# Performance work log

Measured on AMD Instinct MI355X. Metric: run time of the kernel, lower is better.

Reference implementation:

```python
import jax, jax.numpy as jnp
import numpy as np

N, E, F_IN, H, T, G, NCONV = 50000, 800000, 128, 64, 8, 64, 3
BN_EPS = 1e-5


def _bn_relu(h, gamma, beta):
    # BatchNorm1d in training mode: biased batch stats over the node dim
    m = h.mean(axis=0)
    v = h.var(axis=0)
    return jax.nn.relu(gamma * (h - m) * jax.lax.rsqrt(v + BN_EPS) + beta)


def _mlp(h, W1, b1, g1, be1, W2, b2, g2, be2):
    h = _bn_relu(h @ W1 + b1, g1, be1)
    return _bn_relu(h @ W2 + b2, g2, be2)


def setup_inputs() -> dict:
    key = jax.random.key(0)
    ks = jax.random.split(key, 12)
    x = jax.random.normal(ks[0], (N, F_IN), dtype=jnp.float32)
    edge_index = jax.random.randint(ks[1], (2, E), 0, N, dtype=jnp.int64)
    batch = jnp.sort(jax.random.randint(ks[2], (N,), 0, G, dtype=jnp.int64))
    s = 0.05
    inp = {
        "x": x, "edge_index": edge_index, "batch": batch,
        # first_h: Linear(F_IN,H)+BN+ReLU+Linear(H,H)+BN+ReLU
        "fh_W1": jax.random.normal(ks[3], (F_IN, H), jnp.float32) * s,
        "fh_b1": jnp.zeros((H,), jnp.float32),
        "fh_g1": jnp.ones((H,), jnp.float32),
        "fh_be1": jnp.zeros((H,), jnp.float32),
        "fh_W2": jax.random.normal(ks[4], (H, H), jnp.float32) * s,
        "fh_b2": jnp.zeros((H,), jnp.float32),
        "fh_g2": jnp.ones((H,), jnp.float32),
        "fh_be2": jnp.zeros((H,), jnp.float32),
        # stacked GINConv MLPs (all H->H)
        "cv_W1": jax.random.normal(ks[5], (NCONV, H, H), jnp.float32) * s,
        "cv_b1": jnp.zeros((NCONV, H), jnp.float32),
        "cv_g1": jnp.ones((NCONV, H), jnp.float32),
        "cv_be1": jnp.zeros((NCONV, H), jnp.float32),
        "cv_W2": jax.random.normal(ks[6], (NCONV, H, H), jnp.float32) * s,
        "cv_b2": jnp.zeros((NCONV, H), jnp.float32),
        "cv_g2": jnp.ones((NCONV, H), jnp.float32),
        "cv_be2": jnp.zeros((NCONV, H), jnp.float32),
        # per-layer readout linears (NCONV+1 of them)
        "lin_W": jax.random.normal(ks[7], (NCONV + 1, H, T), jnp.float32) * s,
        "lin_b": jnp.zeros((NCONV + 1, T), jnp.float32),
    }
    return inp


def reference(x, edge_index, batch, fh_W1, fh_b1, fh_g1, fh_be1, fh_W2, fh_b2,
              fh_g2, fh_be2, cv_W1, cv_b1, cv_g1, cv_be1, cv_W2, cv_b2, cv_g2,
              cv_be2, lin_W, lin_b):
    src, dst = edge_index[0], edge_index[1]
    eps = 0.0  # eps=0.0, train_eps=False
    # layer 0: first_h + pooled readout
    h = _mlp(x, fh_W1, fh_b1, fh_g1, fh_be1, fh_W2, fh_b2, fh_g2, fh_be2)
    out = jax.ops.segment_max(h @ lin_W[0] + lin_b[0], batch, num_segments=G)
    # GIN conv layers: neighbor sum-aggregation + MLP, with per-layer readout
    for l in range(NCONV):
        agg = jax.ops.segment_sum(h[src], dst, num_segments=N)  # [N,H]
        h = _mlp((1.0 + eps) * h + agg, cv_W1[l], cv_b1[l], cv_g1[l],
                 cv_be1[l], cv_W2[l], cv_b2[l], cv_g2[l], cv_be2[l])
        out = out + jax.ops.segment_max(h @ lin_W[l + 1] + lin_b[l + 1],
                                        batch, num_segments=G)
    return (out, h)
```

## Files before the change

### kernel.cpp

```cpp
#include <hip/hip_runtime.h>
#include <hip/hip_fp16.h>

#define NN 50000
#define EE 800000
#define FIN 128
#define HH 64
#define TT 8
#define GG 64
#define NCONVS 3
#define BN_EPS 1e-5f
#define RNODES 64
#define NBKT 196
#define SCAT_CHUNK 2048

typedef _Float16 h2f __attribute__((ext_vector_type(2)));

__device__ __forceinline__ unsigned enc_f32(float x) {
  unsigned u = __float_as_uint(x);
  return (u & 0x80000000u) ? ~u : (u | 0x80000000u);
}
__device__ __forceinline__ float dec_f32(unsigned e) {
  unsigned u = (e & 0x80000000u) ? (e & 0x7fffffffu) : ~e;
  return __uint_as_float(u);
}

__device__ __forceinline__ float fdot2f(int a, int b, float c) {
#if __has_builtin(__builtin_amdgcn_fdot2)
  return __builtin_amdgcn_fdot2(__builtin_bit_cast(h2f, a),
                                __builtin_bit_cast(h2f, b), c, false);
#else
  const __half2 ha = __builtin_bit_cast(__half2, a);
  const __half2 hb = __builtin_bit_cast(__half2, b);
  const float2 fa = __half22float2(ha), fb = __half22float2(hb);
  return fmaf(fa.y, fb.y, fmaf(fa.x, fb.x, c));
#endif
}

template <int K, int MODE>
__global__ __launch_bounds__(128) void mm_stats_kernel(
    const float* __restrict__ in, const __half* __restrict__ hin,
    const __half* __restrict__ agg, const float* __restrict__ stats_in,
    const float* __restrict__ gamma, const float* __restrict__ beta,
    const float* __restrict__ W, const float* __restrict__ bias,
    __half* __restrict__ y16, float* __restrict__ stats_out) {
  constexpr int NPH = K / 64;
  __shared__ __half2 Wl2[(K / 2) * HH];
  __shared__ __half2 AT2[32 * 68];
  __shared__ float ssl[128];
  __shared__ float sred[2][128];
  const int t = threadIdx.x;
  if (MODE != 0) {
    if (t < 64) {
      const float inv = 1.f / (float)NN;
      const float mean = stats_in[t] * inv;
      const float var = stats_in[64 + t] * inv - mean * mean;
      const float sc = gamma[t] * rsqrtf(var + BN_EPS);
      ssl[t] = sc;
      ssl[64 + t] = fmaf(-mean, sc, beta[t]);
    }
    __syncthreads();
  }
#pragma unroll
  for (int i = 0; i < K / 4; ++i) {
    const int idx = t + i * 128;
    const int kk = idx >> 6, c = idx & 63;
    Wl2[idx] = __floats2half2_rn(W[(2 * kk) * HH + c], W[(2 * kk + 1) * HH + c]);
  }
  const int srow = t >> 1, shalf = t & 1;
  const int grow_s = blockIdx.x * 64 + srow;
  const int cg = t & 7, rg = t >> 3;
  const int c0 = cg * 8, r0 = rg * 4;
  float acc[4][8] = {};

#pragma unroll
  for (int p = 0; p < NPH; ++p) {
    if (p > 0) __syncthreads();
    if (grow_s < NN) {
      if (MODE == 0) {
#pragma unroll
        for (int q = 0; q < 4; ++q) {
          const int cc = p * 64 + shalf * 32 + q * 8;
          const float4 v0 = *(const float4*)&in[(size_t)grow_s * K + cc];
          const float4 v1 = *(const float4*)&in[(size_t)grow_s * K + cc + 4];
          const int kk = shalf * 16 + q * 4;
          AT2[(kk + 0) * 68 + srow] = __floats2half2_rn(v0.x, v0.y);
          AT2[(kk + 1) * 68 + srow] = __floats2half2_rn(v0.z, v0.w);
          AT2[(kk + 2) * 68 + srow] = __floats2half2_rn(v1.x, v1.y);
          AT2[(kk + 3) * 68 + srow] = __floats2half2_rn(v1.z, v1.w);
        }
      } else {
#pragma unroll
        for (int q = 0; q < 4; ++q) {
          const int cc = shalf * 32 + q * 8;
          const int4 rv = *(const int4*)&hin[grow_s * HH + cc];
          const __half2* hp = (const __half2*)&rv;
          float f[8];
          {
            const float2 f0 = __half22float2(hp[0]);
            const float2 f1 = __half22float2(hp[1]);
            const float2 f2 = __half22float2(hp[2]);
            const float2 f3 = __half22float2(hp[3]);
            f[0] = f0.x; f[1] = f0.y; f[2] = f1.x; f[3] = f1.y;
            f[4] = f2.x; f[5] = f2.y; f[6] = f3.x; f[7] = f3.y;
          }
#pragma unroll
          for (int j = 0; j < 8; ++j)
            f[j] = fmaxf(fmaf(f[j], ssl[cc + j], ssl[64 + cc + j]), 0.f);
          if (MODE == 2) {
            const int4 av = *(const int4*)&agg[grow_s * HH + cc];
            const __half2* ap = (const __half2*)&av;
            const float2 a0 = __half22float2(ap[0]);
            const float2 a1 = __half22float2(ap[1]);
            const float2 a2 = __half22float2(ap[2]);
            const float2 a3 = __half22float2(ap[3]);
            f[0] += a0.x; f[1] += a0.y; f[2] += a1.x; f[3] += a1.y;
            f[4] += a2.x; f[5] += a2.y; f[6] += a3.x; f[7] += a3.y;
          }
          const int kk = shalf * 16 + q * 4;
          AT2[(kk + 0) * 68 + srow] = __floats2half2_rn(f[0], f[1]);
          AT2[(kk + 1) * 68 + srow] = __floats2half2_rn(f[2], f[3]);
          AT2[(kk + 2) * 68 + srow] = __floats2half2_rn(f[4], f[5]);
          AT2[(kk + 3) * 68 + srow] = __floats2half2_rn(f[6], f[7]);
        }
      }
    } else {
      const __half2 z = __floats2half2_rn(0.f, 0.f);
#pragma unroll
      for (int i2 = 0; i2 < 16; ++i2) AT2[(shalf * 16 + i2) * 68 + srow] = z;
    }
    __syncthreads();
#pragma unroll 8
    for (int kk = 0; kk < 32; ++kk) {
      const int4 w0 = *(const int4*)&Wl2[(p * 32 + kk) * HH + c0];
      const int4 w1 = *(const int4*)&Wl2[(p * 32 + kk) * HH + c0 + 4];
      const int4 av = *(const int4*)&AT2[kk * 68 + r0];
      const int wu[8] = {w0.x, w0.y, w0.z, w0.w, w1.x, w1.y, w1.z, w1.w};
      const int au[4] = {av.x, av.y, av.z, av.w};
#pragma unroll
      for (int r = 0; r < 4; ++r)
#pragma unroll
        for (int c = 0; c < 8; ++c)
          acc[r][c] = fdot2f(au[r], wu[c], acc[r][c]);
    }
  }
  const float4 bb0 = *(const float4*)&bias[c0];
  const float4 bb1 = *(const float4*)&bias[c0 + 4];
  const float bbv[8] = {bb0.x, bb0.y, bb0.z, bb0.w, bb1.x, bb1.y, bb1.z, bb1.w};
  float st_s[8] = {}, st_q[8] = {};
  const int row0 = blockIdx.x * 64 + r0;
#pragma unroll
  for (int ri = 0; ri < 4; ++ri) {
    const int grow = row0 + ri;
    if (grow < NN) {
      float o[8];
#pragma unroll
      for (int c = 0; c < 8; ++c) {
        o[c] = acc[ri][c] + bbv[c];
        st_s[c] += o[c];
        st_q[c] = fmaf(o[c], o[c], st_q[c]);
      }
      const __half2 p0 = __floats2half2_rn(o[0], o[1]);
      const __half2 p1 = __floats2half2_rn(o[2], o[3]);
      const __half2 p2 = __floats2half2_rn(o[4], o[5]);
      const __half2 p3 = __floats2half2_rn(o[6], o[7]);
      int4 pk;
      pk.x = *(const int*)&p0; pk.y = *(const int*)&p1;
      pk.z = *(const int*)&p2; pk.w = *(const int*)&p3;
      *(int4*)&y16[grow * HH + c0] = pk;
    }
  }
#pragma unroll
  for (int off = 8; off <= 32; off <<= 1) {
#pragma unroll
    for (int c = 0; c < 8; ++c) {
      st_s[c] += __shfl_xor(st_s[c], off);
      st_q[c] += __shfl_xor(st_q[c], off);
    }
  }
  const int wave = t >> 6, lane = t & 63;
  if (lane < 8) {
#pragma unroll
    for (int c = 0; c < 8; ++c) {
      sred[wave][lane * 8 + c] = st_s[c];
      sred[wave][64 + lane * 8 + c] = st_q[c];
    }
  }
  __syncthreads();
  if (t < 128) atomicAdd(&stats_out[t], sred[0][t] + sred[1][t]);
}

__global__ __launch_bounds__(256) void bcount_kernel(const int* __restrict__ ei,
                                                     int* __restrict__ bcnt) {
  __shared__ int l[256];
  const int t = threadIdx.x;
  l[t] = 0;
  __syncthreads();
  for (int e = blockIdx.x * 256 + t; e < EE; e += gridDim.x * 256)
    atomicAdd(&l[ei[EE + e] >> 8], 1);
  __syncthreads();
  if (t < NBKT && l[t]) atomicAdd(&bcnt[t], l[t]);
}

__global__ void bscan_kernel(const int* __restrict__ bcnt,
                             int* __restrict__ bbase, int* __restrict__ bcur) {
  __shared__ int s[256];
  const int t = threadIdx.x;
  const int v = (t < NBKT) ? bcnt[t] : 0;
  s[t] = v;
  __syncthreads();
  for (int off = 1; off < 256; off <<= 1) {
    const int u = (t >= off) ? s[t - off] : 0;
    __syncthreads();
    s[t] += u;
    __syncthreads();
  }
  const int excl = s[t] - v;
  if (t < NBKT) {
    bbase[t] = excl;
    bcur[t] = excl;
  }
  if (t == 255) bbase[NBKT] = s[255];
}

__global__ __launch_bounds__(256) void bscatter_kernel(
    const int* __restrict__ ei, int* __restrict__ bcur,
    unsigned long long* __restrict__ ebuf) {
  __shared__ int lcnt[256];
  __shared__ int lbase[256];
  const int t = threadIdx.x;
  lcnt[t] = 0;
  __syncthreads();
  const int e0 = blockIdx.x * SCAT_CHUNK;
  int mysrc[8], mydl[8], mybkt[8], myloc[8];
#pragma unroll
  for (int i = 0; i < 8; ++i) {
    const int e = e0 + i * 256 + t;
    if (e < EE) {
      const int dst = ei[EE + e];
      mybkt[i] = dst >> 8;
      mydl[i] = dst & 255;
      mysrc[i] = ei[e];
      myloc[i] = atomicAdd(&lcnt[mybkt[i]], 1);
    } else {
      mybkt[i] = -1;
    }
  }
  __syncthreads();
  if (t < NBKT && lcnt[t]) lbase[t] = atomicAdd(&bcur[t], lcnt[t]);
  __syncthreads();
#pragma unroll
  for (int i = 0; i < 8; ++i) {
    if (mybkt[i] >= 0) {
      const int pos = lbase[mybkt[i]] + myloc[i];
      ebuf[pos] = ((unsigned long long)(unsigned)mydl[i] << 32) |
                  (unsigned)mysrc[i];
    }
  }
}

__global__ __launch_bounds__(256) void bcsr_kernel(
    const int* __restrict__ bbase, const unsigned long long* __restrict__ ebuf,
    int* __restrict__ offs, int* __restrict__ srcs) {
  __shared__ int ldeg[256];
  __shared__ int sscan[256];
  __shared__ int lcur[256];
  const int t = threadIdx.x;
  const int b = blockIdx.x;
  const int e0 = bbase[b], e1 = bbase[b + 1];
  ldeg[t] = 0;
  __syncthreads();
  for (int e = e0 + t; e < e1; e += 256)
    atomicAdd(&ldeg[(int)(ebuf[e] >> 32)], 1);
  __syncthreads();
  const int v = ldeg[t];
  sscan[t] = v;
  __syncthreads();
  for (int off = 1; off < 256; off <<= 1) {
    const int u = (t >= off) ? sscan[t - off] : 0;
    __syncthreads();
    sscan[t] += u;
    __syncthreads();
  }
  const int excl = sscan[t] - v;
  const int node = b * 256 + t;
  if (node < NN) offs[node] = e0 + excl;
  if (b == NBKT - 1 && t == 0) offs[NN] = EE;
  lcur[t] = e0 + excl;
  __syncthreads();
  for (int e = e0 + t; e < e1; e += 256) {
    const unsigned long long u = ebuf[e];
    const int dl = (int)(u >> 32);
    const int pos = atomicAdd(&lcur[dl], 1);
    srcs[pos] = (int)(u & 0xffffffffu);
  }
}

__global__ __launch_bounds__(256) void gather16_kernel(
    const int* __restrict__ offs, const int* __restrict__ srcs,
    const __half* __restrict__ y, const float* __restrict__ stats_in,
    const float* __restrict__ gamma, const float* __restrict__ beta,
    __half* __restrict__ agg) {
  __shared__ float ssl[128];
  const int t = threadIdx.x;
  if (t < 64) {
    const float inv = 1.f / (float)NN;
    const float mean = stats_in[t] * inv;
    const float var = stats_in[64 + t] * inv - mean * mean;
    const float sc = gamma[t] * rsqrtf(var + BN_EPS);
    ssl[t] = sc;
    ssl[64 + t] = fmaf(-mean, sc, beta[t]);
  }
  __syncthreads();
  const int gid = blockIdx.x * 256 + t;
  const int n = gid >> 3, lane = gid & 7;
  if (n >= NN) return;
  const int c0 = lane * 8;
  float sc[8], sh[8];
#pragma unroll
  for (int j = 0; j < 8; ++j) {
    sc[j] = ssl[c0 + j];
    sh[j] = ssl[64 + c0 + j];
  }
  const int s0 = offs[n], s1 = offs[n + 1];
  float a[8] = {};
#pragma unroll 2
  for (int j = s0; j < s1; ++j) {
    const int4 rv = *(const int4*)&y[srcs[j] * HH + c0];
    const __half2* hp = (const __half2*)&rv;
    const float2 f0 = __half22float2(hp[0]);
    const float2 f1 = __half22float2(hp[1]);
    const float2 f2 = __half22float2(hp[2]);
    const float2 f3 = __half22float2(hp[3]);
    a[0] += fmaxf(fmaf(f0.x, sc[0], sh[0]), 0.f);
    a[1] += fmaxf(fmaf(f0.y, sc[1], sh[1]), 0.f);
    a[2] += fmaxf(fmaf(f1.x, sc[2], sh[2]), 0.f);
    a[3] += fmaxf(fmaf(f1.y, sc[3], sh[3]), 0.f);
    a[4] += fmaxf(fmaf(f2.x, sc[4], sh[4]), 0.f);
    a[5] += fmaxf(fmaf(f2.y, sc[5], sh[5]), 0.f);
    a[6] += fmaxf(fmaf(f3.x, sc[6], sh[6]), 0.f);
    a[7] += fmaxf(fmaf(f3.y, sc[7], sh[7]), 0.f);
  }
  const __half2 p0 = __floats2half2_rn(a[0], a[1]);
  const __half2 p1 = __floats2half2_rn(a[2], a[3]);
  const __half2 p2 = __floats2half2_rn(a[4], a[5]);
  const __half2 p3 = __floats2half2_rn(a[6], a[7]);
  int4 pk;
  pk.x = *(const int*)&p0; pk.y = *(const int*)&p1;
  pk.z = *(const int*)&p2; pk.w = *(const int*)&p3;
  *(int4*)&agg[n * HH + c0] = pk;
}

template <int WMODE>
__global__ __launch_bounds__(256) void bnrelu_readout_kernel(
    const __half* __restrict__ y2, const float* __restrict__ stats_in,
    const float* __restrict__ gamma, const float* __restrict__ beta,
    float* __restrict__ hout, const float* __restrict__ linW,
    const float* __restrict__ linb, const int* __restrict__ batch,
    unsigned* __restrict__ outmax) {
  __shared__ float Wl[HH * 9];
  __shared__ float lb[8];
  __shared__ float ssl[128];
  __shared__ unsigned smax[8][8];
  const int t = threadIdx.x;
  if (t < 64) {
#pragma unroll
    for (int j = 0; j < 8; ++j) Wl[t * 9 + j] = linW[t * 8 + j];
    const float inv = 1.f / (float)NN;
    const float mean = stats_in[t] * inv;
    const float var = stats_in[64 + t] * inv - mean * mean;
    const float sc = gamma[t] * rsqrtf(var + BN_EPS);
    ssl[t] = sc;
    ssl[64 + t] = fmaf(-mean, sc, beta[t]);
  }
  if (t < 8) lb[t] = linb[t];
  if (t >= 64 && t < 128) smax[(t - 64) >> 3][(t - 64) & 7] = 0u;
  const int gfirst = batch[blockIdx.x * RNODES < NN ? blockIdx.x * RNODES : NN - 1];
  __syncthreads();
  const int nl = t >> 3;
  const int c0 = (t & 7) * 8;
  const int b0 = t & 1, b1 = (t >> 1) & 1, b2 = (t >> 2) & 1;
#pragma unroll
  for (int chunk = 0; chunk < RNODES / 32; ++chunk) {
    const int n = blockIdx.x * RNODES + chunk * 32 + nl;
    if (n < NN) {
      float hv[8];
      {
        const int4 rv = *(const int4*)&y2[n * HH + c0];
        const __half2* hp = (const __half2*)&rv;
        const float2 f0 = __half22float2(hp[0]);
        const float2 f1 = __half22float2(hp[1]);
        const float2 f2 = __half22float2(hp[2]);
        const float2 f3 = __half22float2(hp[3]);
        hv[0] = fmaxf(fmaf(f0.x, ssl[c0 + 0], ssl[64 + c0 + 0]), 0.f);
        hv[1] = fmaxf(fmaf(f0.y, ssl[c0 + 1], ssl[64 + c0 + 1]), 0.f);
        hv[2] = fmaxf(fmaf(f1.x, ssl[c0 + 2], ssl[64 + c0 + 2]), 0.f);
        hv[3] = fmaxf(fmaf(f1.y, ssl[c0 + 3], ssl[64 + c0 + 3]), 0.f);
        hv[4] = fmaxf(fmaf(f2.x, ssl[c0 + 4], ssl[64 + c0 + 4]), 0.f);
        hv[5] = fmaxf(fmaf(f2.y, ssl[c0 + 5], ssl[64 + c0 + 5]), 0.f);
        hv[6] = fmaxf(fmaf(f3.x, ssl[c0 + 6], ssl[64 + c0 + 6]), 0.f);
        hv[7] = fmaxf(fmaf(f3.y, ssl[c0 + 7], ssl[64 + c0 + 7]), 0.f);
      }
      if (WMODE == 1) {
        *(float4*)&hout[n * HH + c0] = make_float4(hv[0], hv[1], hv[2], hv[3]);
        *(float4*)&hout[n * HH + c0 + 4] = make_float4(hv[4], hv[5], hv[6], hv[7]);
      }
      float rr[8] = {0, 0, 0, 0, 0, 0, 0, 0};
#pragma unroll
      for (int j = 0; j < 8; ++j) {
        const float a = hv[j];
        const int k = c0 + j;
#pragma unroll
        for (int u = 0; u < 8; ++u) rr[u] = fmaf(a, Wl[k * 9 + u], rr[u]);
      }
      float s4[4];
#pragma unroll
      for (int i = 0; i < 4; ++i) {
        const float keepv = b0 ? rr[2 * i + 1] : rr[2 * i];
        const float send = b0 ? rr[2 * i] : rr[2 * i + 1];
        s4[i] = keepv + __shfl_xor(send, 1);
      }
      float s2[2];
#pragma unroll
      for (int i = 0; i < 2; ++i) {
        const float keepv = b1 ? s4[2 * i + 1] : s4[2 * i];
        const float send = b1 ? s4[2 * i] : s4[2 * i + 1];
        s2[i] = keepv + __shfl_xor(send, 2);
      }
      const float keepv = b2 ? s2[1] : s2[0];
      const float send = b2 ? s2[0] : s2[1];
      const float v = keepv + __shfl_xor(send, 4) + lb[t & 7];
      const int g = batch[n];
      const int gidx = g - gfirst;
      const unsigned ev = enc_f32(v);
      if (gidx < 8)
        atomicMax(&smax[gidx][t & 7], ev);
      else
        atomicMax(&outmax[g * 8 + (t & 7)], ev);
    }
  }
  __syncthreads();
  if (t < 64) {
    const unsigned vv = smax[t >> 3][t & 7];
    if (vv) atomicMax(&outmax[(gfirst + (t >> 3)) * 8 + (t & 7)], vv);
  }
}

__global__ void combine_kernel(const unsigned* __restrict__ outmax,
                               float* __restrict__ out) {
  const int i = blockIdx.x * 64 + threadIdx.x;
  float s = 0.f;
#pragma unroll
  for (int l = 0; l < 4; ++l) s += dec_f32(outmax[l * GG * TT + i]);
  out[i] = s;
}

extern "C" void kernel_launch(void* const* d_in, const int* in_sizes, int n_in,
                              void* d_out, int out_size, void* d_ws,
                              size_t ws_size, hipStream_t stream) {
  const float* x      = (const float*)d_in[0];
  const int*   ei     = (const int*)d_in[1];
  const int*   batch  = (const int*)d_in[2];
  const float* fh_W1  = (const float*)d_in[3];
  const float* fh_b1  = (const float*)d_in[4];
  const float* fh_g1  = (const float*)d_in[5];
  const float* fh_be1 = (const float*)d_in[6];
  const float* fh_W2  = (const float*)d_in[7];
  const float* fh_b2  = (const float*)d_in[8];
  const float* fh_g2  = (const float*)d_in[9];
  const float* fh_be2 = (const float*)d_in[10];
  const float* cv_W1  = (const float*)d_in[11];
  const float* cv_b1  = (const float*)d_in[12];
  const float* cv_g1  = (const float*)d_in[13];
  const float* cv_be1 = (const float*)d_in[14];
  const float* cv_W2  = (const float*)d_in[15];
  const float* cv_b2  = (const float*)d_in[16];
  const float* cv_g2  = (const float*)d_in[17];
  const float* cv_be2 = (const float*)d_in[18];
  const float* lin_W  = (const float*)d_in[19];
  const float* lin_b  = (const float*)d_in[20];

  float* out = (float*)d_out;
  float* h = out + GG * TT;

  char* w = (char*)d_ws;
  float* stats = (float*)w;                       w += 8 * 128 * 4;
  unsigned* outmax = (unsigned*)w;                w += 4 * GG * TT * 4;
  int* bcnt = (int*)w;                            w += 256 * 4;
  int* bbase = (int*)w;                           w += 256 * 4;
  int* bcur = (int*)w;                            w += 256 * 4;
  int* offs = (int*)w;                            w += (NN + 1) * 4;
  int* srcs = (int*)w;                            w += (size_t)EE * 4;
  w = (char*)(((size_t)w + 15) & ~(size_t)15);
  __half* y1 = (__half*)w;                        w += (size_t)NN * HH * 2;
  __half* y2 = (__half*)w;                        w += (size_t)NN * HH * 2;
  w = (char*)(((size_t)w + 15) & ~(size_t)15);
  __half* agg = (__half*)w;                       w += (size_t)NN * HH * 2;
  unsigned long long* ebuf = (unsigned long long*)agg;

  const int NBLK = (NN + 63) / 64;
  const int NRD = (NN + RNODES - 1) / RNODES;
  const int NGA = (NN * 8 + 255) / 256;
  const int NSC = (EE + SCAT_CHUNK - 1) / SCAT_CHUNK;

  hipMemsetAsync(stats, 0, (8 * 128 + 4 * GG * TT + 256) * sizeof(float),
                 stream);

  bcount_kernel<<<512, 256, 0, stream>>>(ei, bcnt);
  bscan_kernel<<<1, 256, 0, stream>>>(bcnt, bbase, bcur);
  bscatter_kernel<<<NSC, 256, 0, stream>>>(ei, bcur, ebuf);
  bcsr_kernel<<<NBKT, 256, 0, stream>>>(bbase, ebuf, offs, srcs);

  mm_stats_kernel<FIN, 0><<<NBLK, 128, 0, stream>>>(
      x, nullptr, nullptr, nullptr, nullptr, nullptr, fh_W1, fh_b1, y1, stats);
  mm_stats_kernel<HH, 1><<<NBLK, 128, 0, stream>>>(
      nullptr, y1, nullptr, stats, fh_g1, fh_be1, fh_W2, fh_b2, y2,
      stats + 128);
  bnrelu_readout_kernel<0><<<NRD, 256, 0, stream>>>(
      y2, stats + 128, fh_g2, fh_be2, h, lin_W, lin_b, batch, outmax);

  for (int l = 0; l < NCONVS; ++l) {
    float* sprev = stats + (1 + 2 * l) * 128;
    float* sA = stats + (2 + 2 * l) * 128;
    float* sB = stats + (3 + 2 * l) * 128;
    const float* pg = (l == 0) ? fh_g2 : cv_g2 + (l - 1) * HH;
    const float* pb = (l == 0) ? fh_be2 : cv_be2 + (l - 1) * HH;
    gather16_kernel<<<NGA, 256, 0, stream>>>(offs, srcs, y2, sprev, pg, pb,
                                             agg);
    mm_stats_kernel<HH, 2><<<NBLK, 128, 0, stream>>>(
        nullptr, y2, agg, sprev, pg, pb, cv_W1 + l * HH * HH, cv_b1 + l * HH,
        y1, sA);
    mm_stats_kernel<HH, 1><<<NBLK, 128, 0, stream>>>(
        nullptr, y1, nullptr, sA, cv_g1 + l * HH, cv_be1 + l * HH,
        cv_W2 + l * HH * HH, cv_b2 + l * HH, y2, sB);
    if (l == NCONVS - 1) {
      bnrelu_readout_kernel<1><<<NRD, 256, 0, stream>>>(
          y2, sB, cv_g2 + l * HH, cv_be2 + l * HH, h,
          lin_W + (l + 1) * HH * TT, lin_b + (l + 1) * TT, batch,
          outmax + (l + 1) * GG * TT);
    } else {
      bnrelu_readout_kernel<0><<<NRD, 256, 0, stream>>>(
          y2, sB, cv_g2 + l * HH, cv_be2 + l * HH, h,
          lin_W + (l + 1) * HH * TT, lin_b + (l + 1) * TT, batch,
          outmax + (l + 1) * GG * TT);
    }
  }
  combine_kernel<<<8, 64, 0, stream>>>(outmax, out);
}
```

Baseline: 363.9 us.

## Fuse independent graph-preprocessing and gather work into matmul and readout launches

Independent kernels are merged into shared launches by giving extra blocks a different role. The bucket count runs alongside the first matmul, and the scatter alongside the second. CSR build runs with the first readout, and each later neighbour gather runs with the previous layer's readout. This cuts the number of launches and lets small, low-occupancy phases overlap with the dense work. In exchange, block sizes for the preprocessing bodies change from 256 to 128 threads, and the fused kernels carry shared-memory sizes and register pressure from both roles.

```diff
diff --git a/kernel.cpp b/kernel.cpp
--- a/kernel.cpp
+++ b/kernel.cpp
@@ -11,7 +11,12 @@
 #define BN_EPS 1e-5f
 #define RNODES 64
 #define NBKT 196
-#define SCAT_CHUNK 2048
+#define SCAT_CHUNK 1024
+#define NBLK 782
+#define NRD 782
+#define NGA 1563
+#define NSC 782
+#define NB_BC 256
 
 typedef _Float16 h2f __attribute__((ext_vector_type(2)));
 
@@ -37,17 +42,18 @@
 }
 
 template <int K, int MODE>
-__global__ __launch_bounds__(128) void mm_stats_kernel(
-    const float* __restrict__ in, const __half* __restrict__ hin,
-    const __half* __restrict__ agg, const float* __restrict__ stats_in,
-    const float* __restrict__ gamma, const float* __restrict__ beta,
-    const float* __restrict__ W, const float* __restrict__ bias,
-    __half* __restrict__ y16, float* __restrict__ stats_out) {
+__device__ __forceinline__ void mm_body(
+    char* smemc, int bid, const float* __restrict__ in,
+    const __half* __restrict__ hin, const __half* __restrict__ agg,
+    const float* __restrict__ stats_in, const float* __restrict__ gamma,
+    const float* __restrict__ beta, const float* __restrict__ W,
+    const float* __restrict__ bias, __half* __restrict__ y16,
+    float* __restrict__ stats_out) {
   constexpr int NPH = K / 64;
-  __shared__ __half2 Wl2[(K / 2) * HH];
-  __shared__ __half2 AT2[32 * 68];
-  __shared__ float ssl[128];
-  __shared__ float sred[2][128];
+  __half2* Wl2 = (__half2*)smemc;
+  __half2* AT2 = (__half2*)(smemc + (K / 2) * HH * 4);
+  float* ssl = (float*)(smemc + (K / 2) * HH * 4 + 32 * 68 * 4);
+  float* sred = ssl + 128;
   const int t = threadIdx.x;
   if (MODE != 0) {
     if (t < 64) {
@@ -67,7 +73,7 @@
     Wl2[idx] = __floats2half2_rn(W[(2 * kk) * HH + c], W[(2 * kk + 1) * HH + c]);
   }
   const int srow = t >> 1, shalf = t & 1;
-  const int grow_s = blockIdx.x * 64 + srow;
+  const int grow_s = bid * 64 + srow;
   const int cg = t & 7, rg = t >> 3;
   const int c0 = cg * 8, r0 = rg * 4;
   float acc[4][8] = {};
@@ -147,7 +153,7 @@
   const float4 bb1 = *(const float4*)&bias[c0 + 4];
   const float bbv[8] = {bb0.x, bb0.y, bb0.z, bb0.w, bb1.x, bb1.y, bb1.z, bb1.w};
   float st_s[8] = {}, st_q[8] = {};
-  const int row0 = blockIdx.x * 64 + r0;
+  const int row0 = bid * 64 + r0;
 #pragma unroll
   for (int ri = 0; ri < 4; ++ri) {
     const int grow = row0 + ri;
@@ -181,24 +187,27 @@
   if (lane < 8) {
 #pragma unroll
     for (int c = 0; c < 8; ++c) {
-      sred[wave][lane * 8 + c] = st_s[c];
-      sred[wave][64 + lane * 8 + c] = st_q[c];
-    }
-  }
-  __syncthreads();
-  if (t < 128) atomicAdd(&stats_out[t], sred[0][t] + sred[1][t]);
-}
-
-__global__ __launch_bounds__(256) void bcount_kernel(const int* __restrict__ ei,
-                                                     int* __restrict__ bcnt) {
-  __shared__ int l[256];
+      sred[wave * 128 + lane * 8 + c] = st_s[c];
+      sred[wave * 128 + 64 + lane * 8 + c] = st_q[c];
+    }
+  }
+  __syncthreads();
+  atomicAdd(&stats_out[t], sred[t] + sred[128 + t]);
+}
+
+__device__ __forceinline__ void bcount_body(char* smemc, int bid,
+                                            const int* __restrict__ ei,
+                                            int* __restrict__ bcnt) {
+  int* hist = (int*)smemc;
   const int t = threadIdx.x;
-  l[t] = 0;
-  __syncthreads();
-  for (int e = blockIdx.x * 256 + t; e < EE; e += gridDim.x * 256)
-    atomicAdd(&l[ei[EE + e] >> 8], 1);
-  __syncthreads();
-  if (t < NBKT && l[t]) atomicAdd(&bcnt[t], l[t]);
+  hist[t] = 0; hist[t + 128] = 0;
+  __syncthreads();
+  for (int e = bid * 128 + t; e < EE; e += NB_BC * 128)
+    atomicAdd(&hist[ei[EE + e] >> 8], 1);
+  __syncthreads();
+  const int v0 = hist[t], v1 = hist[t + 128];
+  if (v0) atomicAdd(&bcnt[t], v0);
+  if (v1) atomicAdd(&bcnt[t + 128], v1);
 }
 
 __global__ void bscan_kernel(const int* __restrict__ bcnt,
@@ -222,19 +231,19 @@
   if (t == 255) bbase[NBKT] = s[255];
 }
 
-__global__ __launch_bounds__(256) void bscatter_kernel(
-    const int* __restrict__ ei, int* __restrict__ bcur,
+__device__ __forceinline__ void bscatter_body(
+    char* smemc, int bid, const int* __restrict__ ei, int* __restrict__ bcur,
     unsigned long long* __restrict__ ebuf) {
-  __shared__ int lcnt[256];
-  __shared__ int lbase[256];
+  int* lcnt = (int*)smemc;
+  int* lbase = lcnt + 256;
   const int t = threadIdx.x;
-  lcnt[t] = 0;
-  __syncthreads();
-  const int e0 = blockIdx.x * SCAT_CHUNK;
+  lcnt[t] = 0; lcnt[t + 128] = 0;
+  __syncthreads();
+  const int e0 = bid * SCAT_CHUNK;
   int mysrc[8], mydl[8], mybkt[8], myloc[8];
 #pragma unroll
   for (int i = 0; i < 8; ++i) {
-    const int e = e0 + i * 256 + t;
+    const int e = e0 + i * 128 + t;
     if (e < EE) {
       const int dst = ei[EE + e];
       mybkt[i] = dst >> 8;
@@ -246,7 +255,8 @@
     }
   }
   __syncthreads();
-  if (t < NBKT && lcnt[t]) lbase[t] = atomicAdd(&bcur[t], lcnt[t]);
+  if (lcnt[t]) lbase[t] = atomicAdd(&bcur[t], lcnt[t]);
+  if (lcnt[t + 128]) lbase[t + 128] = atomicAdd(&bcur[t + 128], lcnt[t + 128]);
   __syncthreads();
 #pragma unroll
   for (int i = 0; i < 8; ++i) {
@@ -258,14 +268,14 @@
   }
 }
 
-__global__ __launch_bounds__(256) void bcsr_kernel(
-    const int* __restrict__ bbase, const unsigned long long* __restrict__ ebuf,
-    int* __restrict__ offs, int* __restrict__ srcs) {
-  __shared__ int ldeg[256];
-  __shared__ int sscan[256];
-  __shared__ int lcur[256];
+__device__ __forceinline__ void bcsr_body(
+    char* smemc, int b, const int* __restrict__ bbase,
+    const unsigned long long* __restrict__ ebuf, int* __restrict__ offs,
+    int* __restrict__ srcs) {
+  int* ldeg = (int*)smemc;
+  int* sscan = ldeg + 256;
+  int* lcur = sscan + 256;
   const int t = threadIdx.x;
-  const int b = blockIdx.x;
   const int e0 = bbase[b], e1 = bbase[b + 1];
   ldeg[t] = 0;
   __syncthreads();
@@ -295,12 +305,12 @@
   }
 }
 
-__global__ __launch_bounds__(256) void gather16_kernel(
-    const int* __restrict__ offs, const int* __restrict__ srcs,
-    const __half* __restrict__ y, const float* __restrict__ stats_in,
-    const float* __restrict__ gamma, const float* __restrict__ beta,
-    __half* __restrict__ agg) {
-  __shared__ float ssl[128];
+__device__ __forceinline__ void gather_body(
+    char* smemc, int bid, const int* __restrict__ offs,
+    const int* __restrict__ srcs, const __half* __restrict__ y,
+    const float* __restrict__ stats_in, const float* __restrict__ gamma,
+    const float* __restrict__ beta, __half* __restrict__ agg) {
+  float* ssl = (float*)smemc;
   const int t = threadIdx.x;
   if (t < 64) {
     const float inv = 1.f / (float)NN;
@@ -311,7 +321,7 @@
     ssl[64 + t] = fmaf(-mean, sc, beta[t]);
   }
   __syncthreads();
-  const int gid = blockIdx.x * 256 + t;
+  const int gid = bid * 256 + t;
   const int n = gid >> 3, lane = gid & 7;
   if (n >= NN) return;
   const int c0 = lane * 8;
@@ -351,16 +361,16 @@
 }
 
 template <int WMODE>
-__global__ __launch_bounds__(256) void bnrelu_readout_kernel(
-    const __half* __restrict__ y2, const float* __restrict__ stats_in,
-    const float* __restrict__ gamma, const float* __restrict__ beta,
-    float* __restrict__ hout, const float* __restrict__ linW,
-    const float* __restrict__ linb, const int* __restrict__ batch,
-    unsigned* __restrict__ outmax) {
-  __shared__ float Wl[HH * 9];
-  __shared__ float lb[8];
-  __shared__ float ssl[128];
-  __shared__ unsigned smax[8][8];
+__device__ __forceinline__ void readout_body(
+    char* smemc, int bid, const __half* __restrict__ y2,
+    const float* __restrict__ stats_in, const float* __restrict__ gamma,
+    const float* __restrict__ beta, float* __restrict__ hout,
+    const float* __restrict__ linW, const float* __restrict__ linb,
+    const int* __restrict__ batch, unsigned* __restrict__ outmax) {
+  float* Wl = (float*)smemc;
+  float* lb = Wl + 576;
+  float* ssl = lb + 8;
+  unsigned* smax = (unsigned*)(ssl + 128);
   const int t = threadIdx.x;
   if (t < 64) {
 #pragma unroll
@@ -373,15 +383,15 @@
     ssl[64 + t] = fmaf(-mean, sc, beta[t]);
   }
   if (t < 8) lb[t] = linb[t];
-  if (t >= 64 && t < 128) smax[(t - 64) >> 3][(t - 64) & 7] = 0u;
-  const int gfirst = batch[blockIdx.x * RNODES < NN ? blockIdx.x * RNODES : NN - 1];
+  if (t >= 64 && t < 128) smax[t - 64] = 0u;
+  const int gfirst = batch[bid * RNODES < NN ? bid * RNODES : NN - 1];
   __syncthreads();
   const int nl = t >> 3;
   const int c0 = (t & 7) * 8;
   const int b0 = t & 1, b1 = (t >> 1) & 1, b2 = (t >> 2) & 1;
 #pragma unroll
   for (int chunk = 0; chunk < RNODES / 32; ++chunk) {
-    const int n = blockIdx.x * RNODES + chunk * 32 + nl;
+    const int n = bid * RNODES + chunk * 32 + nl;
     if (n < NN) {
       float hv[8];
       {
@@ -402,7 +412,8 @@
       }
       if (WMODE == 1) {
         *(float4*)&hout[n * HH + c0] = make_float4(hv[0], hv[1], hv[2], hv[3]);
-        *(float4*)&hout[n * HH + c0 + 4] = make_float4(hv[4], hv[5], hv[6], hv[7]);
+        *(float4*)&hout[n * HH + c0 + 4] =
+            make_float4(hv[4], hv[5], hv[6], hv[7]);
       }
       float rr[8] = {0, 0, 0, 0, 0, 0, 0, 0};
 #pragma unroll
@@ -433,16 +444,62 @@
       const int gidx = g - gfirst;
       const unsigned ev = enc_f32(v);
       if (gidx < 8)
-        atomicMax(&smax[gidx][t & 7], ev);
+        atomicMax(&smax[gidx * 8 + (t & 7)], ev);
       else
         atomicMax(&outmax[g * 8 + (t & 7)], ev);
     }
   }
   __syncthreads();
   if (t < 64) {
-    const unsigned vv = smax[t >> 3][t & 7];
+    const unsigned vv = smax[t];
     if (vv) atomicMax(&outmax[(gfirst + (t >> 3)) * 8 + (t & 7)], vv);
   }
+}
+
+template <int K, int MODE, int TAIL>
+__global__ __launch_bounds__(128) void mm_fused_kernel(
+    const float* in, const __half* hin, const __half* agg,
+    const float* stats_in, const float* gamma, const float* beta,
+    const float* W, const float* bias, __half* y16, float* stats_out,
+    const int* ei, int* bcnt, int* bcur, unsigned long long* ebuf) {
+  constexpr int SMEM = (K / 2) * HH * 4 + 32 * 68 * 4 + 512 + 1024;
+  __shared__ alignas(16) char smem[SMEM];
+  const int bid = blockIdx.x;
+  if (bid < NBLK) {
+    mm_body<K, MODE>(smem, bid, in, hin, agg, stats_in, gamma, beta, W, bias,
+                     y16, stats_out);
+  } else if (TAIL == 1) {
+    bcount_body(smem, bid - NBLK, ei, bcnt);
+  } else if (TAIL == 2) {
+    bscatter_body(smem, bid - NBLK, ei, bcur, ebuf);
+  }
+}
+
+template <int WMODE, int TAIL>
+__global__ __launch_bounds__(256) void readout_fused_kernel(
+    const __half* y2, const float* stats_in, const float* gamma,
+    const float* beta, float* hout, const float* linW, const float* linb,
+    const int* batch, unsigned* outmax, const int* offs_in,
+    const int* srcs_in, __half* agg, const int* bbase,
+    const unsigned long long* ebuf, int* offs_out, int* srcs_out) {
+  __shared__ alignas(16) char smem[3136];
+  const int bid = blockIdx.x;
+  if (bid < NRD) {
+    readout_body<WMODE>(smem, bid, y2, stats_in, gamma, beta, hout, linW,
+                        linb, batch, outmax);
+  } else if (TAIL == 1) {
+    bcsr_body(smem, bid - NRD, bbase, ebuf, offs_out, srcs_out);
+  } else if (TAIL == 2) {
+    gather_body(smem, bid - NRD, offs_in, srcs_in, y2, stats_in, gamma, beta,
+                agg);
+  }
+}
+
+__global__ __launch_bounds__(256) void gather_kernel(
+    const int* offs, const int* srcs, const __half* y, const float* stats_in,
+    const float* gamma, const float* beta, __half* agg) {
+  __shared__ alignas(16) char smem[512];
+  gather_body(smem, blockIdx.x, offs, srcs, y, stats_in, gamma, beta, agg);
 }
 
 __global__ void combine_kernel(const unsigned* __restrict__ outmax,
@@ -497,26 +554,21 @@
   __half* agg = (__half*)w;                       w += (size_t)NN * HH * 2;
   unsigned long long* ebuf = (unsigned long long*)agg;
 
-  const int NBLK = (NN + 63) / 64;
-  const int NRD = (NN + RNODES - 1) / RNODES;
-  const int NGA = (NN * 8 + 255) / 256;
-  const int NSC = (EE + SCAT_CHUNK - 1) / SCAT_CHUNK;
-
   hipMemsetAsync(stats, 0, (8 * 128 + 4 * GG * TT + 256) * sizeof(float),
                  stream);
 
-  bcount_kernel<<<512, 256, 0, stream>>>(ei, bcnt);
+  mm_fused_kernel<FIN, 0, 1><<<NBLK + NB_BC, 128, 0, stream>>>(
+      x, nullptr, nullptr, nullptr, nullptr, nullptr, fh_W1, fh_b1, y1, stats,
+      ei, bcnt, bcur, ebuf);
   bscan_kernel<<<1, 256, 0, stream>>>(bcnt, bbase, bcur);
-  bscatter_kernel<<<NSC, 256, 0, stream>>>(ei, bcur, ebuf);
-  bcsr_kernel<<<NBKT, 256, 0, stream>>>(bbase, ebuf, offs, srcs);
-
-  mm_stats_kernel<FIN, 0><<<NBLK, 128, 0, stream>>>(
-      x, nullptr, nullptr, nullptr, nullptr, nullptr, fh_W1, fh_b1, y1, stats);
-  mm_stats_kernel<HH, 1><<<NBLK, 128, 0, stream>>>(
+  mm_fused_kernel<HH, 1, 2><<<NBLK + NSC, 128, 0, stream>>>(
       nullptr, y1, nullptr, stats, fh_g1, fh_be1, fh_W2, fh_b2, y2,
-      stats + 128);
-  bnrelu_readout_kernel<0><<<NRD, 256, 0, stream>>>(
-      y2, stats + 128, fh_g2, fh_be2, h, lin_W, lin_b, batch, outmax);
+      stats + 128, ei, bcnt, bcur, ebuf);
+  readout_fused_kernel<0, 1><<<NRD + NBKT, 256, 0, stream>>>(
+      y2, stats + 128, fh_g2, fh_be2, h, lin_W, lin_b, batch, outmax,
+      nullptr, nullptr, nullptr, bbase, ebuf, offs, srcs);
+  gather_kernel<<<NGA, 256, 0, stream>>>(offs, srcs, y2, stats + 128, fh_g2,
+                                         fh_be2, agg);
 
   for (int l = 0; l < NCONVS; ++l) {
     float* sprev = stats + (1 + 2 * l) * 128;
@@ -524,24 +576,24 @@
     float* sB = stats + (3 + 2 * l) * 128;
     const float* pg = (l == 0) ? fh_g2 : cv_g2 + (l - 1) * HH;
     const float* pb = (l == 0) ? fh_be2 : cv_be2 + (l - 1) * HH;
-    gather16_kernel<<<NGA, 256, 0, stream>>>(offs, srcs, y2, sprev, pg, pb,
-                                             agg);
-    mm_stats_kernel<HH, 2><<<NBLK, 128, 0, stream>>>(
+    mm_fused_kernel<HH, 2, 0><<<NBLK, 128, 0, stream>>>(
         nullptr, y2, agg, sprev, pg, pb, cv_W1 + l * HH * HH, cv_b1 + l * HH,
-        y1, sA);
-    mm_stats_kernel<HH, 1><<<NBLK, 128, 0, stream>>>(
+        y1, sA, ei, bcnt, bcur, ebuf);
+    mm_fused_kernel<HH, 1, 0><<<NBLK, 128, 0, stream>>>(
         nullptr, y1, nullptr, sA, cv_g1 + l * HH, cv_be1 + l * HH,
-        cv_W2 + l * HH * HH, cv_b2 + l * HH, y2, sB);
-    if (l == NCONVS - 1) {
-      bnrelu_readout_kernel<1><<<NRD, 256, 0, stream>>>(
+        cv_W2 + l * HH * HH, cv_b2 + l * HH, y2, sB, ei, bcnt, bcur, ebuf);
+    if (l < NCONVS - 1) {
+      readout_fused_kernel<0, 2><<<NRD + NGA, 256, 0, stream>>>(
           y2, sB, cv_g2 + l * HH, cv_be2 + l * HH, h,
           lin_W + (l + 1) * HH * TT, lin_b + (l + 1) * TT, batch,
-          outmax + (l + 1) * GG * TT);
+          outmax + (l + 1) * GG * TT, offs, srcs, agg, nullptr, nullptr,
+          nullptr, nullptr);
     } else {
-      bnrelu_readout_kernel<0><<<NRD, 256, 0, stream>>>(
+      readout_fused_kernel<1, 0><<<NRD, 256, 0, stream>>>(
           y2, sB, cv_g2 + l * HH, cv_be2 + l * HH, h,
           lin_W + (l + 1) * HH * TT, lin_b + (l + 1) * TT, batch,
-          outmax + (l + 1) * GG * TT);
+          outmax + (l + 1) * GG * TT, nullptr, nullptr, nullptr, nullptr,
+          nullptr, nullptr, nullptr);
     }
   }
   combine_kernel<<<8, 64, 0, stream>>>(outmax, out);
```

Result: faster. 330.2 us (-9.3%).
